# Optimization experiments

Measured on AMD Instinct MI355X. Metric: run time of the kernel, lower is better.

Reference implementation:

```python
import jax, jax.numpy as jnp
import numpy as np

B, FEAT, SPD_H, CTRL_H, N_CMD = 32768, 512, 128, 256, 4


def _p(key, shape, fan_in):
    # torch nn.Linear default init: U(-1/sqrt(fan_in), 1/sqrt(fan_in))
    lim = 1.0 / np.sqrt(fan_in)
    return jax.random.uniform(key, shape, jnp.float32, -lim, lim)


def setup_inputs() -> dict:
    key = jax.random.key(0)
    ks = iter(jax.random.split(key, 32))
    inp = {
        "feat": jax.random.normal(next(ks), (B, FEAT), jnp.float32),
        "speed": jax.random.uniform(next(ks), (B,), jnp.float32),
        "command": jax.random.randint(next(ks), (B,), 0, N_CMD, jnp.int32),
        "ms_w1": _p(next(ks), (1, SPD_H), 1), "ms_b1": _p(next(ks), (SPD_H,), 1),
        "ms_w2": _p(next(ks), (SPD_H, SPD_H), SPD_H), "ms_b2": _p(next(ks), (SPD_H,), SPD_H),
        "ms_w3": _p(next(ks), (SPD_H, SPD_H), SPD_H), "ms_b3": _p(next(ks), (SPD_H,), SPD_H),
        # speed_pred_module: 512 -> 256 -> 256 -> 1
        "sp_w1": _p(next(ks), (FEAT, CTRL_H), FEAT), "sp_b1": _p(next(ks), (CTRL_H,), FEAT),
        "sp_w2": _p(next(ks), (CTRL_H, CTRL_H), CTRL_H), "sp_b2": _p(next(ks), (CTRL_H,), CTRL_H),
        "sp_w3": _p(next(ks), (CTRL_H, 1), CTRL_H), "sp_b3": _p(next(ks), (1,), CTRL_H),
        # join_module: Linear(640, 512)
        "join_w": _p(next(ks), (FEAT + SPD_H, FEAT), FEAT + SPD_H),
        "join_b": _p(next(ks), (FEAT,), FEAT + SPD_H),
        # 4 control heads: 512 -> 256 -> 256 -> 3 (stacked on expert axis e)
        "ctrl_w1": _p(next(ks), (N_CMD, FEAT, CTRL_H), FEAT), "ctrl_b1": _p(next(ks), (N_CMD, CTRL_H), FEAT),
        "ctrl_w2": _p(next(ks), (N_CMD, CTRL_H, CTRL_H), CTRL_H), "ctrl_b2": _p(next(ks), (N_CMD, CTRL_H), CTRL_H),
        "ctrl_w3": _p(next(ks), (N_CMD, CTRL_H, 3), CTRL_H), "ctrl_b3": _p(next(ks), (N_CMD, 3), CTRL_H),
    }
    return inp


def _mlp(x, w1, b1, w2, b2, w3, b3):
    # FullyConnectedNet: Linear, ReLU, Linear, Dropout(p=0 -> noop), ReLU, Linear
    h = jax.nn.relu(x @ w1 + b1)
    h = jax.nn.relu(h @ w2 + b2)
    return h @ w3 + b3


def reference(feat, speed, command,
              ms_w1, ms_b1, ms_w2, ms_b2, ms_w3, ms_b3,
              sp_w1, sp_b1, sp_w2, sp_b2, sp_w3, sp_b3,
              join_w, join_b,
              ctrl_w1, ctrl_b1, ctrl_w2, ctrl_b2, ctrl_w3, ctrl_b3):
    v = _mlp(speed[:, None], ms_w1, ms_b1, ms_w2, ms_b2, ms_w3, ms_b3)      # [B,128]
    joined = jnp.concatenate([feat, v], axis=1) @ join_w + join_b           # [B,512]
    v_p = _mlp(feat, sp_w1, sp_b1, sp_w2, sp_b2, sp_w3, sp_b3)              # [B,1]
    # command-indexed dispatch: compute all 4 heads densely, then select per sample
    h1 = jax.nn.relu(jnp.einsum('bd,edh->beh', joined, ctrl_w1) + ctrl_b1)  # [B,4,256]
    h2 = jax.nn.relu(jnp.einsum('beh,ehk->bek', h1, ctrl_w2) + ctrl_b2)     # [B,4,256]
    act_all = jnp.einsum('bek,eko->beo', h2, ctrl_w3) + ctrl_b3             # [B,4,3]
    action = jnp.take_along_axis(act_all, command[:, None, None].astype(jnp.int32), axis=1)[:, 0]  # [B,3]
    throttle = jax.nn.sigmoid(action[:, 0])
    steering = jnp.tanh(action[:, 1])
    brake = jax.nn.sigmoid(action[:, 2])
    return v_p, throttle, brake, steering
```

## Files before the change

kernel.cpp:

```cpp
#include <hip/hip_runtime.h>
#include <hip/hip_bf16.h>
#include <stdint.h>
#include <math.h>

#define BB 32768
#define FEAT 512
#define SPD_H 128
#define CTRL_H 256
#define NCMD 4

typedef __attribute__((ext_vector_type(8))) short bf16x8;
typedef __attribute__((ext_vector_type(4))) float f32x4;

__device__ __forceinline__ unsigned short f2bf(float f) {
  union { float f; uint32_t u; } v; v.f = f;
  uint32_t u = v.u;
  return (unsigned short)((u + 0x7fffu + ((u >> 16) & 1u)) >> 16);
}

__device__ __forceinline__ bf16x8 pack8(float4 a, float4 b) {
  bf16x8 r;
  r[0] = (short)f2bf(a.x); r[1] = (short)f2bf(a.y);
  r[2] = (short)f2bf(a.z); r[3] = (short)f2bf(a.w);
  r[4] = (short)f2bf(b.x); r[5] = (short)f2bf(b.y);
  r[6] = (short)f2bf(b.z); r[7] = (short)f2bf(b.w);
  return r;
}

__device__ __forceinline__ void async16(const unsigned short* g, unsigned short* l) {
  __builtin_amdgcn_global_load_lds(
      (const __attribute__((address_space(1))) unsigned int*)g,
      (__attribute__((address_space(3))) unsigned int*)l, 16, 0, 0);
}

__device__ __forceinline__ void gemm128(
    const unsigned short* __restrict__ A, int lda,
    const int* __restrict__ perm, int m_start, int m_cnt,
    const unsigned short* __restrict__ W, const float* __restrict__ bi,
    unsigned short* __restrict__ C, int ldc, int relu, int K, int mt, int nt) {
  extern __shared__ __align__(16) unsigned char dynsm[];
  unsigned short* As = (unsigned short*)dynsm;
  unsigned short* Bs = As + 128 * 32;

  const int m0 = mt * 128;
  if (m0 >= m_cnt) return;
  const int n0 = nt * 128;
  const int t = threadIdx.x;
  const int w = t >> 6, lane = t & 63;
  const int wm = w & 1, wn = w >> 1;

  f32x4 acc[4][4];
#pragma unroll
  for (int i = 0; i < 4; ++i)
#pragma unroll
    for (int j = 0; j < 4; ++j)
#pragma unroll
      for (int r = 0; r < 4; ++r) acc[i][j][r] = 0.f;

  const int fr = lane & 15;
  const int fk = (lane >> 4) * 8;

  const unsigned short* agp[2]; const unsigned short* bgp[2];
  unsigned short* al[2]; unsigned short* bl[2];
#pragma unroll
  for (int it = 0; it < 2; ++it) {
    int row = w * 32 + it * 16 + (lane >> 2);
    int seg8 = (lane & 3) * 8;
    int rl = m0 + row;
    if (rl >= m_cnt) rl = m_cnt - 1;
    int grow = perm ? perm[m_start + rl] : (m_start + rl);
    agp[it] = A + (size_t)grow * lda + seg8;
    bgp[it] = W + (size_t)(n0 + row) * K + seg8;
    al[it] = As + (w * 32 + it * 16) * 32;
    bl[it] = Bs + (w * 32 + it * 16) * 32;
  }

  for (int k0 = 0; k0 < K; k0 += 32) {
#pragma unroll
    for (int it = 0; it < 2; ++it) {
      async16(agp[it] + k0, al[it]);
      async16(bgp[it] + k0, bl[it]);
    }
    __syncthreads();
    bf16x8 af[4], bfv[4];
#pragma unroll
    for (int i = 0; i < 4; ++i)
      af[i] = *(const bf16x8*)(As + (wm * 64 + i * 16 + fr) * 32 + fk);
#pragma unroll
    for (int j = 0; j < 4; ++j)
      bfv[j] = *(const bf16x8*)(Bs + (wn * 64 + j * 16 + fr) * 32 + fk);
#pragma unroll
    for (int i = 0; i < 4; ++i)
#pragma unroll
      for (int j = 0; j < 4; ++j)
        acc[i][j] = __builtin_amdgcn_mfma_f32_16x16x32_bf16(af[i], bfv[j], acc[i][j], 0, 0, 0);
    __syncthreads();
  }

  const int rquad = (lane >> 4) * 4;
  const int cidx = lane & 15;

  float bv[4];
#pragma unroll
  for (int j = 0; j < 4; ++j) bv[j] = bi ? bi[n0 + wn * 64 + j * 16 + cidx] : 0.f;

  unsigned short (*bscr)[136] = (unsigned short(*)[136])dynsm;
#pragma unroll
  for (int c = 0; c < 4; ++c) {
    if (wm == (c >> 1)) {
#pragma unroll
      for (int j = 0; j < 4; ++j) {
#pragma unroll
        for (int ii = 0; ii < 2; ++ii) {
          int i = 2 * (c & 1) + ii;
          int lr = ii * 16 + rquad;
#pragma unroll
          for (int r = 0; r < 4; ++r) {
            float v = acc[i][j][r] + bv[j];
            if (relu) v = fmaxf(v, 0.f);
            bscr[lr + r][wn * 64 + j * 16 + cidx] = f2bf(v);
          }
        }
      }
    }
    __syncthreads();
#pragma unroll
    for (int q = 0; q < 2; ++q) {
      int sg = t + 256 * q;
      int lr = sg >> 4, cs = (sg & 15) * 8;
      int grow = m0 + c * 32 + lr;
      if (grow < m_cnt)
        *(bf16x8*)(C + (size_t)(m_start + grow) * ldc + (n0 + cs)) =
            *(const bf16x8*)(&bscr[lr][cs]);
    }
    __syncthreads();
  }
}

struct WSeg { const float* src; unsigned short* dst; int K; int N; int ldd; };
struct PrepArgs {
  WSeg s[12];
  int start[13];
  const float* join_w; unsigned short* wjbf;
  const int* cmd; int* wavecnt;
  const float* join_b; const float* ctrl_w1; const float* ctrl_b1; float* b_f;
};
__launch_bounds__(256)
__global__ void k_prep(PrepArgs a) {
  int bx = blockIdx.x, t = threadIdx.x;
  if (bx < 320) {
    int idx = bx * 256 + t;
    float4 f = *(const float4*)(a.join_w + (size_t)idx * 4);
    ushort4 o;
    o.x = f2bf(f.x); o.y = f2bf(f.y); o.z = f2bf(f.z); o.w = f2bf(f.w);
    *(ushort4*)(a.wjbf + (size_t)idx * 4) = o;
    return;
  }
  int rel = bx - 320;
  if (rel < a.start[12]) {
    __shared__ float tb[32][33];
    int si = 0;
    while (rel >= a.start[si + 1]) ++si;
    WSeg sg = a.s[si];
    int tile = rel - a.start[si];
    int tkx = sg.K >> 5;
    int tn = tile / tkx;
    int tk = tile - tn * tkx;
    int k0 = tk * 32, n0 = tn * 32;
    int tx = t & 31, ty = t >> 5;
#pragma unroll
    for (int j = 0; j < 4; ++j)
      tb[ty + j * 8][tx] = sg.src[(size_t)(k0 + ty + j * 8) * sg.N + n0 + tx];
    __syncthreads();
#pragma unroll
    for (int j = 0; j < 4; ++j)
      sg.dst[(size_t)(n0 + ty + j * 8) * sg.ldd + k0 + tx] = f2bf(tb[tx][ty + j * 8]);
    return;
  }
  rel -= a.start[12];
  if (rel < 128) {
    int i = rel * 256 + t;
    int c = a.cmd[i];
    int wid = i >> 6;
    int lane = t & 63;
#pragma unroll
    for (int cv = 0; cv < NCMD; ++cv) {
      unsigned long long m = __ballot(c == cv);
      if (lane == 0) a.wavecnt[cv * 512 + wid] = __popcll(m);
    }
    return;
  }
  int e = rel - 128;
  float s0 = a.ctrl_b1[e * 256 + t], s1 = 0.f, s2 = 0.f, s3 = 0.f;
  const float* w = a.ctrl_w1 + (size_t)e * 512 * 256 + t;
#pragma unroll 4
  for (int m = 0; m < 512; m += 4) {
    s0 = fmaf(a.join_b[m + 0], w[(size_t)(m + 0) * 256], s0);
    s1 = fmaf(a.join_b[m + 1], w[(size_t)(m + 1) * 256], s1);
    s2 = fmaf(a.join_b[m + 2], w[(size_t)(m + 2) * 256], s2);
    s3 = fmaf(a.join_b[m + 3], w[(size_t)(m + 3) * 256], s3);
  }
  a.b_f[e * 256 + t] = (s0 + s1) + (s2 + s3);
}

struct MidArgs {
  const int* cmd; const int* wavecnt; int* perm; int* offs;
  const unsigned short* c_w1t; const unsigned short* wjbf; unsigned short* wf_t;
  const float* speed;
  const float* ms_w1; const float* ms_b1;
  const unsigned short* ms_w2t; const float* ms_b2;
  const unsigned short* ms_w3t; const float* ms_b3;
  unsigned short* msout;
  int* tile_e; int* tile_r0; int* ntl;
};
__launch_bounds__(256)
__global__ void k_mid(MidArgs a) {
  int b = blockIdx.x, t = threadIdx.x;
  if (b >= 168) {
    extern __shared__ __align__(16) unsigned char dynsm[];
    unsigned short (*hw)[136] = (unsigned short(*)[136])dynsm;
    unsigned short* BsM = (unsigned short*)(dynsm + 128 * 136 * 2);
    const int m0 = (b - 168) * 128;
    const int w = t >> 6, lane = t & 63;
    const int wm = w & 1, wn = w >> 1;
    const int fr = lane & 15, fk = (lane >> 4) * 8;
    const int rquad = (lane >> 4) * 4, cidx = lane & 15;
    {
      int r = t >> 1, half = t & 1;
      float s = a.speed[m0 + r];
#pragma unroll
      for (int c0 = 0; c0 < 64; c0 += 4) {
        int c = half * 64 + c0;
        float4 wv = *(const float4*)(a.ms_w1 + c);
        float4 bv = *(const float4*)(a.ms_b1 + c);
        hw[r][c + 0] = f2bf(fmaxf(fmaf(s, wv.x, bv.x), 0.f));
        hw[r][c + 1] = f2bf(fmaxf(fmaf(s, wv.y, bv.y), 0.f));
        hw[r][c + 2] = f2bf(fmaxf(fmaf(s, wv.z, bv.z), 0.f));
        hw[r][c + 3] = f2bf(fmaxf(fmaf(s, wv.w, bv.w), 0.f));
      }
    }
    __syncthreads();
    for (int layer = 0; layer < 2; ++layer) {
      const unsigned short* Wt = layer ? a.ms_w3t : a.ms_w2t;
      const float* bb = layer ? a.ms_b3 : a.ms_b2;
      f32x4 acc[4][4];
#pragma unroll
      for (int i = 0; i < 4; ++i)
#pragma unroll
        for (int j = 0; j < 4; ++j)
#pragma unroll
          for (int r = 0; r < 4; ++r) acc[i][j][r] = 0.f;
      for (int k0 = 0; k0 < 128; k0 += 32) {
#pragma unroll
        for (int it = 0; it < 2; ++it) {
          int row = w * 32 + it * 16 + (lane >> 2);
          async16(Wt + (size_t)row * 128 + k0 + (lane & 3) * 8,
                  BsM + (w * 32 + it * 16) * 32);
        }
        __syncthreads();
        bf16x8 af[4], bfv[4];
#pragma unroll
        for (int i = 0; i < 4; ++i)
          af[i] = *(const bf16x8*)(&hw[wm * 64 + i * 16 + fr][k0 + fk]);
#pragma unroll
        for (int j = 0; j < 4; ++j)
          bfv[j] = *(const bf16x8*)(BsM + (wn * 64 + j * 16 + fr) * 32 + fk);
#pragma unroll
        for (int i = 0; i < 4; ++i)
#pragma unroll
          for (int j = 0; j < 4; ++j)
            acc[i][j] = __builtin_amdgcn_mfma_f32_16x16x32_bf16(af[i], bfv[j], acc[i][j], 0, 0, 0);
        __syncthreads();
      }
#pragma unroll
      for (int j = 0; j < 4; ++j) {
        int col = wn * 64 + j * 16 + cidx;
        float bv = bb[col];
#pragma unroll
        for (int i = 0; i < 4; ++i) {
          int row = wm * 64 + i * 16 + rquad;
#pragma unroll
          for (int r = 0; r < 4; ++r) {
            float v = acc[i][j][r] + bv;
            if (layer == 0) v = fmaxf(v, 0.f);
            hw[row + r][col] = f2bf(v);
          }
        }
      }
      __syncthreads();
    }
    {
      int r = t >> 1, half = t & 1;
#pragma unroll
      for (int c8 = 0; c8 < 8; ++c8)
        *(bf16x8*)(a.msout + (size_t)(m0 + r) * 128 + half * 64 + c8 * 8) =
            *(const bf16x8*)(&hw[r][half * 64 + c8 * 8]);
    }
    return;
  }
  if (b >= 128) {
    int idx = b - 128;
    int mt = idx & 7, nt = idx >> 3;
    gemm128(a.c_w1t, 512, nullptr, 0, 1024, a.wjbf, nullptr, a.wf_t, 640, 0, 512, mt, nt);
    return;
  }
  __shared__ int pf[NCMD][4];
  __shared__ int tot[NCMD];
  int c = t >> 6, lane = t & 63;
  int v[8]; int s = 0;
#pragma unroll
  for (int q = 0; q < 8; ++q) { v[q] = a.wavecnt[c * 512 + lane * 8 + q]; s += v[q]; }
  int p = s;
#pragma unroll
  for (int m = 1; m < 64; m <<= 1) { int o = __shfl_up(p, m, 64); if (lane >= m) p += o; }
  int excl = p - s;
  if (lane == 63) tot[c] = p;
  if (lane == ((4 * b) >> 3)) {
    int base_off = (4 * b) & 7;
    int run = excl;
#pragma unroll
    for (int q = 0; q < 8; ++q) {
      if (q >= base_off && q < base_off + 4) pf[c][q - base_off] = run;
      run += v[q];
    }
  }
  __syncthreads();
  int soffs[NCMD + 1];
  soffs[0] = 0;
#pragma unroll
  for (int e = 0; e < NCMD; ++e) soffs[e + 1] = soffs[e] + tot[e];
  if (b == 0 && t == 0)
    for (int e = 0; e <= NCMD; ++e) a.offs[e] = soffs[e];
  int i = b * 256 + t;
  int mc = a.cmd[i];
  int lwid = t >> 6;
  int rank = 0, base = 0;
#pragma unroll
  for (int cv = 0; cv < NCMD; ++cv) {
    unsigned long long m = __ballot(mc == cv);
    if (mc == cv) {
      rank = __popcll(m & ((1ull << lane) - 1ull));
      base = soffs[cv] + pf[cv][lwid];
    }
  }
  a.perm[base + rank] = i;

  if (b == 0) {
    int toff[NCMD + 1];
    toff[0] = 0;
#pragma unroll
    for (int ee = 0; ee < NCMD; ++ee) toff[ee + 1] = toff[ee] + ((tot[ee] + 63) >> 6);
    if (t == 0) a.ntl[0] = toff[NCMD];
    for (int ti = t; ti < toff[NCMD]; ti += 256) {
      int ee = 0;
      while (ti >= toff[ee + 1]) ++ee;
      a.tile_e[ti] = ee;
      a.tile_r0[ti] = soffs[ee] + (ti - toff[ee]) * 64;
    }
  }
}

struct TailArgs {
  const float* feat;
  const unsigned short* msout;
  const unsigned short* wf_t;  const float* b_f;
  const unsigned short* sp_w1t; const float* sp_b1;
  const unsigned short* c_w2t; const float* ctrl_b2;
  const unsigned short* sp_w2t; const float* sp_b2;
  const float* ctrl_w3; const float* ctrl_b3;
  const float* sp_w3; const float* sp_b3;
  const int* perm; const int* seg;
  const int* tile_e; const int* tile_r0; const int* ntl;
  float* out;
};
__launch_bounds__(256, 3)
__global__ void k_tail(TailArgs a) {
  extern __shared__ __align__(16) unsigned char dynsm[];
  unsigned short* As = (unsigned short*)dynsm;
  unsigned short* h1 = (unsigned short*)(dynsm + 16384);
  float* pscr = (float*)dynsm;

  const int t = threadIdx.x;
  const int w = t >> 6, lane = t & 63;
  const int fr = lane & 15, fcg = lane >> 4;
  const int rquad = fcg * 4, cidx = fr;
  const int row_s = t >> 2, sl = t & 3;

  int is_sp, e = 0, NC;
  const unsigned short *W1, *W2;
  const float *b1, *b2;
  int r0, rend;
  if (blockIdx.x < 512) {
    is_sp = 1; NC = 8;
    W1 = a.sp_w1t; W2 = a.sp_w2t; b1 = a.sp_b1; b2 = a.sp_b2;
    r0 = blockIdx.x * 64; rend = BB;
  } else {
    int ti = blockIdx.x - 512;
    if (ti >= a.ntl[0]) return;
    is_sp = 0; e = a.tile_e[ti]; NC = 10;
    W1 = a.wf_t + (size_t)e * 256 * 640;
    W2 = a.c_w2t + (size_t)e * 65536;
    b1 = a.b_f + e * 256; b2 = a.ctrl_b2 + e * 256;
    r0 = a.tile_r0[ti]; rend = a.seg[e + 1];
  }
  const int K = is_sp ? 512 : 640;

  const float* fsrc; const unsigned short* msrc;
  {
    int rl = r0 + row_s;
    if (rl >= rend) rl = rend - 1;
    int grow = is_sp ? rl : a.perm[rl];
    fsrc = a.feat + (size_t)grow * 512 + sl * 16;
    msrc = a.msout + (size_t)grow * 128 + sl * 16;
  }
  const int xr = row_s & 7;
  unsigned short* wp0 = As + row_s * 64 + (((2 * sl) ^ xr) << 3);
  unsigned short* wp1 = As + row_s * 64 + (((2 * sl + 1) ^ xr) << 3);

  const unsigned short* bp[4];
#pragma unroll
  for (int j = 0; j < 4; ++j)
    bp[j] = W1 + (size_t)(w * 64 + j * 16 + fr) * K + fcg * 8;

  f32x4 acc[4][4];
#pragma unroll
  for (int i = 0; i < 4; ++i)
#pragma unroll
    for (int j = 0; j < 4; ++j)
#pragma unroll
      for (int r = 0; r < 4; ++r) acc[i][j][r] = 0.f;

  float4 g0, g1, g2, g3; bf16x8 mv0, mv1;

#define LOADA(cc)                                                        \
  do {                                                                   \
    if ((cc) < 8) {                                                      \
      g0 = *(const float4*)(fsrc + (cc) * 64 + 0);                       \
      g1 = *(const float4*)(fsrc + (cc) * 64 + 4);                       \
      g2 = *(const float4*)(fsrc + (cc) * 64 + 8);                       \
      g3 = *(const float4*)(fsrc + (cc) * 64 + 12);                      \
    } else {                                                             \
      mv0 = *(const bf16x8*)(msrc + ((cc) - 8) * 64 + 0);                \
      mv1 = *(const bf16x8*)(msrc + ((cc) - 8) * 64 + 8);                \
    }                                                                    \
  } while (0)

#define WRITEA(cc, bufb)                                                 \
  do {                                                                   \
    bf16x8 s0_, s1_;                                                     \
    if ((cc) < 8) { s0_ = pack8(g0, g1); s1_ = pack8(g2, g3); }          \
    else { s0_ = mv0; s1_ = mv1; }                                       \
    *(bf16x8*)(wp0 + (bufb)) = s0_;                                      \
    *(bf16x8*)(wp1 + (bufb)) = s1_;                                      \
  } while (0)

  LOADA(0);
  WRITEA(0, 0);
  LOADA(1);
  __syncthreads();

  for (int c = 0; c < NC; ++c) {
    const int cr = (c & 1) * 4096;
    if (c + 1 < NC) WRITEA(c + 1, ((c + 1) & 1) * 4096);
    if (c + 2 < NC) LOADA(c + 2);
#pragma unroll
    for (int ks = 0; ks < 2; ++ks) {
      const int k0 = c * 64 + ks * 32;
      bf16x8 af[4], bv[4];
#pragma unroll
      for (int i = 0; i < 4; ++i)
        af[i] = *(const bf16x8*)(As + cr + (i * 16 + fr) * 64 +
                                 (((ks * 4 + fcg) ^ (fr & 7)) << 3));
#pragma unroll
      for (int j = 0; j < 4; ++j)
        bv[j] = *(const bf16x8*)(bp[j] + k0);
#pragma unroll
      for (int i = 0; i < 4; ++i)
#pragma unroll
        for (int j = 0; j < 4; ++j)
          acc[i][j] = __builtin_amdgcn_mfma_f32_16x16x32_bf16(af[i], bv[j], acc[i][j], 0, 0, 0);
    }
    __syncthreads();
  }
#undef LOADA
#undef WRITEA

#pragma unroll
  for (int j = 0; j < 4; ++j) {
    const int col = w * 64 + j * 16 + cidx;
    const float bj = b1[col];
    const int c8 = col >> 3, cl = col & 7;
#pragma unroll
    for (int i = 0; i < 4; ++i) {
#pragma unroll
      for (int r = 0; r < 4; ++r) {
        const int row = i * 16 + rquad + r;
        h1[(row << 8) + (((c8 ^ (row & 7)) << 3) | cl)] =
            f2bf(fmaxf(acc[i][j][r] + bj, 0.f));
      }
    }
  }
  __syncthreads();

  const unsigned short* bp2[4];
#pragma unroll
  for (int j = 0; j < 4; ++j)
    bp2[j] = W2 + (size_t)(w * 64 + j * 16 + fr) * 256 + fcg * 8;

#pragma unroll
  for (int i = 0; i < 4; ++i)
#pragma unroll
    for (int j = 0; j < 4; ++j)
#pragma unroll
      for (int r = 0; r < 4; ++r) acc[i][j][r] = 0.f;

#pragma unroll 2
  for (int k0 = 0; k0 < 256; k0 += 32) {
    bf16x8 af[4], bv[4];
#pragma unroll
    for (int i = 0; i < 4; ++i) {
      const int row = i * 16 + fr;
      const int c8 = (k0 >> 3) + fcg;
      af[i] = *(const bf16x8*)(h1 + (row << 8) + ((c8 ^ (row & 7)) << 3));
    }
#pragma unroll
    for (int j = 0; j < 4; ++j)
      bv[j] = *(const bf16x8*)(bp2[j] + k0);
#pragma unroll
    for (int i = 0; i < 4; ++i)
#pragma unroll
      for (int j = 0; j < 4; ++j)
        acc[i][j] = __builtin_amdgcn_mfma_f32_16x16x32_bf16(af[i], bv[j], acc[i][j], 0, 0, 0);
  }

  float b2v[4], w30[4], w31[4], w32[4];
#pragma unroll
  for (int j = 0; j < 4; ++j) {
    const int col = w * 64 + j * 16 + cidx;
    b2v[j] = b2[col];
    if (is_sp) {
      w30[j] = a.sp_w3[col]; w31[j] = 0.f; w32[j] = 0.f;
    } else {
      const float* wp = a.ctrl_w3 + (size_t)e * 768 + col * 3;
      w30[j] = wp[0]; w31[j] = wp[1]; w32[j] = wp[2];
    }
  }
#pragma unroll
  for (int i = 0; i < 4; ++i) {
#pragma unroll
    for (int r = 0; r < 4; ++r) {
      float s0 = 0.f, s1 = 0.f, s2 = 0.f;
#pragma unroll
      for (int j = 0; j < 4; ++j) {
        const float v = fmaxf(acc[i][j][r] + b2v[j], 0.f);
        s0 = fmaf(v, w30[j], s0);
        if (!is_sp) { s1 = fmaf(v, w31[j], s1); s2 = fmaf(v, w32[j], s2); }
      }
#pragma unroll
      for (int m = 1; m <= 8; m <<= 1) {
        s0 += __shfl_xor(s0, m, 64);
        if (!is_sp) { s1 += __shfl_xor(s1, m, 64); s2 += __shfl_xor(s2, m, 64); }
      }
      if (cidx == 0) {
        const int row = i * 16 + rquad + r;
        pscr[(row * 4 + w) * 3 + 0] = s0;
        if (!is_sp) {
          pscr[(row * 4 + w) * 3 + 1] = s1;
          pscr[(row * 4 + w) * 3 + 2] = s2;
        }
      }
    }
  }
  __syncthreads();

  if (is_sp) {
    if (t < 64) {
      float s = pscr[t * 12] + pscr[t * 12 + 3] + pscr[t * 12 + 6] + pscr[t * 12 + 9]
              + a.sp_b3[0];
      a.out[r0 + t] = s;
    }
  } else {
    if (t < 192) {
      const int row = t / 3, o = t - row * 3;
      const int rl = r0 + row;
      if (rl < rend) {
        float s = pscr[row * 12 + o] + pscr[row * 12 + 3 + o] +
                  pscr[row * 12 + 6 + o] + pscr[row * 12 + 9 + o] +
                  a.ctrl_b3[e * 3 + o];
        const int orig = a.perm[rl];
        if (o == 0)      a.out[BB + orig]     = 1.f / (1.f + __expf(-s));
        else if (o == 2) a.out[2 * BB + orig] = 1.f / (1.f + __expf(-s));
        else             a.out[3 * BB + orig] = tanhf(s);
      }
    }
  }
}

static inline size_t align256(size_t x) { return (x + 255) & ~(size_t)255; }

extern "C" void kernel_launch(void* const* d_in, const int* in_sizes, int n_in,
                              void* d_out, int out_size, void* d_ws, size_t ws_size,
                              hipStream_t stream) {
  const float* feat   = (const float*)d_in[0];
  const float* speed  = (const float*)d_in[1];
  const int*   command= (const int*)d_in[2];
  const float* ms_w1  = (const float*)d_in[3];
  const float* ms_b1  = (const float*)d_in[4];
  const float* ms_w2  = (const float*)d_in[5];
  const float* ms_b2  = (const float*)d_in[6];
  const float* ms_w3  = (const float*)d_in[7];
  const float* ms_b3  = (const float*)d_in[8];
  const float* sp_w1  = (const float*)d_in[9];
  const float* sp_b1  = (const float*)d_in[10];
  const float* sp_w2  = (const float*)d_in[11];
  const float* sp_b2  = (const float*)d_in[12];
  const float* sp_w3  = (const float*)d_in[13];
  const float* sp_b3  = (const float*)d_in[14];
  const float* join_w = (const float*)d_in[15];
  const float* join_b = (const float*)d_in[16];
  const float* ctrl_w1= (const float*)d_in[17];
  const float* ctrl_b1= (const float*)d_in[18];
  const float* ctrl_w2= (const float*)d_in[19];
  const float* ctrl_b2= (const float*)d_in[20];
  const float* ctrl_w3= (const float*)d_in[21];
  const float* ctrl_b3= (const float*)d_in[22];
  float* out = (float*)d_out;

  char* ws = (char*)d_ws;
  size_t off = 0;
  auto alloc = [&](size_t bytes) -> char* { char* p = ws + off; off = align256(off + bytes); return p; };

  unsigned short* msout  = (unsigned short*)alloc((size_t)BB * 128 * 2);
  unsigned short* wtp    = (unsigned short*)alloc(1998848ull * 2);
  int* perm    = (int*)alloc((size_t)BB * 4);
  int* cnt     = (int*)alloc(64);
  int* wavecnt = (int*)alloc(4 * 512 * 4);
  float* b_f   = (float*)alloc(4 * 256 * 4);
  int* tile_e  = (int*)alloc(1056 * 4);
  int* tile_r0 = (int*)alloc(1056 * 4);
  int* ntl     = (int*)alloc(64);

  unsigned short* sp_w1t = wtp;
  unsigned short* sp_w2t = wtp + 131072;
  unsigned short* ms_w2t = wtp + 196608;
  unsigned short* ms_w3t = wtp + 212992;
  unsigned short* c_w1t  = wtp + 229376;
  unsigned short* c_w2t  = wtp + 753664;
  unsigned short* wjbf   = wtp + 1015808;
  unsigned short* wf_t   = wtp + 1343488;

  PrepArgs P;
  P.s[0] = { sp_w1, sp_w1t, 512, 256, 512 };
  P.s[1] = { sp_w2, sp_w2t, 256, 256, 256 };
  P.s[2] = { ms_w2, ms_w2t, 128, 128, 128 };
  P.s[3] = { ms_w3, ms_w3t, 128, 128, 128 };
  for (int e = 0; e < 4; ++e) P.s[4 + e] = { ctrl_w1 + (size_t)e * 512 * 256, c_w1t + (size_t)e * 131072, 512, 256, 512 };
  for (int e = 0; e < 4; ++e) P.s[8 + e] = { ctrl_w2 + (size_t)e * 256 * 256, c_w2t + (size_t)e * 65536, 256, 256, 256 };
  P.start[0] = 0;
  for (int i = 0; i < 12; ++i)
    P.start[i + 1] = P.start[i] + (P.s[i].K >> 5) * (P.s[i].N >> 5);
  P.join_w = join_w; P.wjbf = wjbf;
  P.cmd = command; P.wavecnt = wavecnt;
  P.join_b = join_b; P.ctrl_w1 = ctrl_w1; P.ctrl_b1 = ctrl_b1; P.b_f = b_f;
  int prep_blocks = 320 + P.start[12] + 128 + 4;

  k_prep<<<prep_blocks, 256, 0, stream>>>(P);

  MidArgs Mi;
  Mi.cmd = command; Mi.wavecnt = wavecnt; Mi.perm = perm; Mi.offs = cnt + 4;
  Mi.c_w1t = c_w1t; Mi.wjbf = wjbf; Mi.wf_t = wf_t;
  Mi.speed = speed;
  Mi.ms_w1 = ms_w1; Mi.ms_b1 = ms_b1;
  Mi.ms_w2t = ms_w2t; Mi.ms_b2 = ms_b2;
  Mi.ms_w3t = ms_w3t; Mi.ms_b3 = ms_b3;
  Mi.msout = msout;
  Mi.tile_e = tile_e; Mi.tile_r0 = tile_r0; Mi.ntl = ntl;
  k_mid<<<168 + 256, 256, 128 * 136 * 2 + 128 * 32 * 2, stream>>>(Mi);

  TailArgs T;
  T.feat = feat; T.msout = msout;
  T.wf_t = wf_t; T.b_f = b_f;
  T.sp_w1t = sp_w1t; T.sp_b1 = sp_b1;
  T.c_w2t = c_w2t; T.ctrl_b2 = ctrl_b2;
  T.sp_w2t = sp_w2t; T.sp_b2 = sp_b2;
  T.ctrl_w3 = ctrl_w3; T.ctrl_b3 = ctrl_b3;
  T.sp_w3 = sp_w3; T.sp_b3 = sp_b3;
  T.perm = perm; T.seg = cnt + 4;
  T.tile_e = tile_e; T.tile_r0 = tile_r0; T.ntl = ntl;
  T.out = out;
  k_tail<<<dim3(512 + 516), 256, 49152, stream>>>(T);
}
```

Measured before the change: 230.0 us.

## Fuse speed-pred MLP into control-head tail tiles and split bias fold

The speed-prediction MLP now runs inside each control-head tile instead of in separate blocks. Each tile reuses its staged feat A-tiles for both the control GEMM and the speed-pred GEMM and writes v_p through the permutation. This halves the feat reads and removes 512 blocks from the tail launch. In exchange each block holds two accumulator sets and uses more LDS (80KB), so occupancy drops to 2 blocks per CU. Separately, the join_b·ctrl_w1 bias fold is split into 32 partial blocks whose results k_mid reduces, which shortens the serial tail of k_prep.

```diff
diff --git a/kernel.cpp b/kernel.cpp
--- a/kernel.cpp
+++ b/kernel.cpp
@@ -143,7 +143,7 @@
   int start[13];
   const float* join_w; unsigned short* wjbf;
   const int* cmd; int* wavecnt;
-  const float* join_b; const float* ctrl_w1; const float* ctrl_b1; float* b_f;
+  const float* join_b; const float* ctrl_w1; float* bf_part;
 };
 __launch_bounds__(256)
 __global__ void k_prep(PrepArgs a) {
@@ -190,17 +190,25 @@
     }
     return;
   }
-  int e = rel - 128;
-  float s0 = a.ctrl_b1[e * 256 + t], s1 = 0.f, s2 = 0.f, s3 = 0.f;
-  const float* w = a.ctrl_w1 + (size_t)e * 512 * 256 + t;
-#pragma unroll 4
-  for (int m = 0; m < 512; m += 4) {
-    s0 = fmaf(a.join_b[m + 0], w[(size_t)(m + 0) * 256], s0);
-    s1 = fmaf(a.join_b[m + 1], w[(size_t)(m + 1) * 256], s1);
-    s2 = fmaf(a.join_b[m + 2], w[(size_t)(m + 2) * 256], s2);
-    s3 = fmaf(a.join_b[m + 3], w[(size_t)(m + 3) * 256], s3);
-  }
-  a.b_f[e * 256 + t] = (s0 + s1) + (s2 + s3);
+  int idx = rel - 128;
+  int e = idx >> 3, ch = idx & 7;
+  const float* w = a.ctrl_w1 + (size_t)e * 512 * 256 + (size_t)ch * 64 * 256 + t;
+  const float* jb = a.join_b + ch * 64;
+  float s0 = 0.f, s1 = 0.f, s2 = 0.f, s3 = 0.f;
+  float s4 = 0.f, s5 = 0.f, s6 = 0.f, s7 = 0.f;
+#pragma unroll
+  for (int g = 0; g < 8; ++g) {
+    s0 = fmaf(jb[g * 8 + 0], w[(size_t)(g * 8 + 0) * 256], s0);
+    s1 = fmaf(jb[g * 8 + 1], w[(size_t)(g * 8 + 1) * 256], s1);
+    s2 = fmaf(jb[g * 8 + 2], w[(size_t)(g * 8 + 2) * 256], s2);
+    s3 = fmaf(jb[g * 8 + 3], w[(size_t)(g * 8 + 3) * 256], s3);
+    s4 = fmaf(jb[g * 8 + 4], w[(size_t)(g * 8 + 4) * 256], s4);
+    s5 = fmaf(jb[g * 8 + 5], w[(size_t)(g * 8 + 5) * 256], s5);
+    s6 = fmaf(jb[g * 8 + 6], w[(size_t)(g * 8 + 6) * 256], s6);
+    s7 = fmaf(jb[g * 8 + 7], w[(size_t)(g * 8 + 7) * 256], s7);
+  }
+  a.bf_part[(size_t)(e * 8 + ch) * 256 + t] =
+      ((s0 + s1) + (s2 + s3)) + ((s4 + s5) + (s6 + s7));
 }
 
 struct MidArgs {
@@ -211,11 +219,20 @@
   const unsigned short* ms_w2t; const float* ms_b2;
   const unsigned short* ms_w3t; const float* ms_b3;
   unsigned short* msout;
+  const float* bf_part; const float* ctrl_b1; float* b_f;
   int* tile_e; int* tile_r0; int* ntl;
 };
 __launch_bounds__(256)
 __global__ void k_mid(MidArgs a) {
   int b = blockIdx.x, t = threadIdx.x;
+  if (b >= 424) {
+    int e = b - 424;
+    float s = a.ctrl_b1[e * 256 + t];
+#pragma unroll
+    for (int ch = 0; ch < 8; ++ch) s += a.bf_part[(size_t)(e * 8 + ch) * 256 + t];
+    a.b_f[e * 256 + t] = s;
+    return;
+  }
   if (b >= 168) {
     extern __shared__ __align__(16) unsigned char dynsm[];
     unsigned short (*hw)[136] = (unsigned short(*)[136])dynsm;
@@ -373,12 +390,14 @@
   const int* tile_e; const int* tile_r0; const int* ntl;
   float* out;
 };
-__launch_bounds__(256, 3)
+__launch_bounds__(256, 2)
 __global__ void k_tail(TailArgs a) {
   extern __shared__ __align__(16) unsigned char dynsm[];
-  unsigned short* As = (unsigned short*)dynsm;
-  unsigned short* h1 = (unsigned short*)(dynsm + 16384);
-  float* pscr = (float*)dynsm;
+  unsigned short* As  = (unsigned short*)dynsm;
+  unsigned short* h1c = (unsigned short*)(dynsm + 16384);
+  unsigned short* h1s = (unsigned short*)(dynsm + 49152);
+  float* pscr_c = (float*)dynsm;
+  float* pscr_s = (float*)(dynsm + 4096);
 
   const int t = threadIdx.x;
   const int w = t >> 6, lane = t & 63;
@@ -386,30 +405,21 @@
   const int rquad = fcg * 4, cidx = fr;
   const int row_s = t >> 2, sl = t & 3;
 
-  int is_sp, e = 0, NC;
-  const unsigned short *W1, *W2;
-  const float *b1, *b2;
-  int r0, rend;
-  if (blockIdx.x < 512) {
-    is_sp = 1; NC = 8;
-    W1 = a.sp_w1t; W2 = a.sp_w2t; b1 = a.sp_b1; b2 = a.sp_b2;
-    r0 = blockIdx.x * 64; rend = BB;
-  } else {
-    int ti = blockIdx.x - 512;
-    if (ti >= a.ntl[0]) return;
-    is_sp = 0; e = a.tile_e[ti]; NC = 10;
-    W1 = a.wf_t + (size_t)e * 256 * 640;
-    W2 = a.c_w2t + (size_t)e * 65536;
-    b1 = a.b_f + e * 256; b2 = a.ctrl_b2 + e * 256;
-    r0 = a.tile_r0[ti]; rend = a.seg[e + 1];
-  }
-  const int K = is_sp ? 512 : 640;
+  const int ti = blockIdx.x;
+  if (ti >= a.ntl[0]) return;
+  const int e = a.tile_e[ti];
+  const int r0 = a.tile_r0[ti], rend = a.seg[e + 1];
+
+  const unsigned short* W1c = a.wf_t + (size_t)e * 256 * 640;
+  const unsigned short* W2c = a.c_w2t + (size_t)e * 65536;
+  const float* b1c = a.b_f + e * 256;
+  const float* b2c = a.ctrl_b2 + e * 256;
 
   const float* fsrc; const unsigned short* msrc;
   {
     int rl = r0 + row_s;
     if (rl >= rend) rl = rend - 1;
-    int grow = is_sp ? rl : a.perm[rl];
+    int grow = a.perm[rl];
     fsrc = a.feat + (size_t)grow * 512 + sl * 16;
     msrc = a.msout + (size_t)grow * 128 + sl * 16;
   }
@@ -417,18 +427,21 @@
   unsigned short* wp0 = As + row_s * 64 + (((2 * sl) ^ xr) << 3);
   unsigned short* wp1 = As + row_s * 64 + (((2 * sl + 1) ^ xr) << 3);
 
-  const unsigned short* bp[4];
-#pragma unroll
-  for (int j = 0; j < 4; ++j)
-    bp[j] = W1 + (size_t)(w * 64 + j * 16 + fr) * K + fcg * 8;
-
-  f32x4 acc[4][4];
+  const unsigned short* bpc[4]; const unsigned short* bps[4];
+#pragma unroll
+  for (int j = 0; j < 4; ++j) {
+    const int row = w * 64 + j * 16 + fr;
+    bpc[j] = W1c + (size_t)row * 640 + fcg * 8;
+    bps[j] = a.sp_w1t + (size_t)row * 512 + fcg * 8;
+  }
+
+  f32x4 accC[4][4], accS[4][4];
 #pragma unroll
   for (int i = 0; i < 4; ++i)
 #pragma unroll
     for (int j = 0; j < 4; ++j)
 #pragma unroll
-      for (int r = 0; r < 4; ++r) acc[i][j][r] = 0.f;
+      for (int r = 0; r < 4; ++r) { accC[i][j][r] = 0.f; accS[i][j][r] = 0.f; }
 
   float4 g0, g1, g2, g3; bf16x8 mv0, mv1;
 
@@ -459,10 +472,11 @@
   LOADA(1);
   __syncthreads();
 
-  for (int c = 0; c < NC; ++c) {
+#pragma unroll 2
+  for (int c = 0; c < 10; ++c) {
     const int cr = (c & 1) * 4096;
-    if (c + 1 < NC) WRITEA(c + 1, ((c + 1) & 1) * 4096);
-    if (c + 2 < NC) LOADA(c + 2);
+    if (c + 1 < 10) WRITEA(c + 1, ((c + 1) & 1) * 4096);
+    if (c + 2 < 10) LOADA(c + 2);
 #pragma unroll
     for (int ks = 0; ks < 2; ++ks) {
       const int k0 = c * 64 + ks * 32;
@@ -473,12 +487,23 @@
                                  (((ks * 4 + fcg) ^ (fr & 7)) << 3));
 #pragma unroll
       for (int j = 0; j < 4; ++j)
-        bv[j] = *(const bf16x8*)(bp[j] + k0);
+        bv[j] = *(const bf16x8*)(bpc[j] + k0);
 #pragma unroll
       for (int i = 0; i < 4; ++i)
 #pragma unroll
         for (int j = 0; j < 4; ++j)
-          acc[i][j] = __builtin_amdgcn_mfma_f32_16x16x32_bf16(af[i], bv[j], acc[i][j], 0, 0, 0);
+          accC[i][j] = __builtin_amdgcn_mfma_f32_16x16x32_bf16(af[i], bv[j], accC[i][j], 0, 0, 0);
+      if (c < 8) {
+        bf16x8 bs[4];
+#pragma unroll
+        for (int j = 0; j < 4; ++j)
+          bs[j] = *(const bf16x8*)(bps[j] + k0);
+#pragma unroll
+        for (int i = 0; i < 4; ++i)
+#pragma unroll
+          for (int j = 0; j < 4; ++j)
+            accS[i][j] = __builtin_amdgcn_mfma_f32_16x16x32_bf16(af[i], bs[j], accS[i][j], 0, 0, 0);
+      }
     }
     __syncthreads();
   }
@@ -488,110 +513,122 @@
 #pragma unroll
   for (int j = 0; j < 4; ++j) {
     const int col = w * 64 + j * 16 + cidx;
-    const float bj = b1[col];
+    const float bjc = b1c[col];
+    const float bjs = a.sp_b1[col];
     const int c8 = col >> 3, cl = col & 7;
 #pragma unroll
     for (int i = 0; i < 4; ++i) {
 #pragma unroll
       for (int r = 0; r < 4; ++r) {
         const int row = i * 16 + rquad + r;
-        h1[(row << 8) + (((c8 ^ (row & 7)) << 3) | cl)] =
-            f2bf(fmaxf(acc[i][j][r] + bj, 0.f));
+        const int off = (row << 8) + (((c8 ^ (row & 7)) << 3) | cl);
+        h1c[off] = f2bf(fmaxf(accC[i][j][r] + bjc, 0.f));
+        h1s[off] = f2bf(fmaxf(accS[i][j][r] + bjs, 0.f));
       }
     }
   }
   __syncthreads();
 
-  const unsigned short* bp2[4];
-#pragma unroll
-  for (int j = 0; j < 4; ++j)
-    bp2[j] = W2 + (size_t)(w * 64 + j * 16 + fr) * 256 + fcg * 8;
-
+  const unsigned short* bp2c[4]; const unsigned short* bp2s[4];
+#pragma unroll
+  for (int j = 0; j < 4; ++j) {
+    const int row = w * 64 + j * 16 + fr;
+    bp2c[j] = W2c + (size_t)row * 256 + fcg * 8;
+    bp2s[j] = a.sp_w2t + (size_t)row * 256 + fcg * 8;
+  }
 #pragma unroll
   for (int i = 0; i < 4; ++i)
 #pragma unroll
     for (int j = 0; j < 4; ++j)
 #pragma unroll
-      for (int r = 0; r < 4; ++r) acc[i][j][r] = 0.f;
+      for (int r = 0; r < 4; ++r) { accC[i][j][r] = 0.f; accS[i][j][r] = 0.f; }
 
 #pragma unroll 2
   for (int k0 = 0; k0 < 256; k0 += 32) {
-    bf16x8 af[4], bv[4];
+    bf16x8 afc[4], afs[4], bv[4], bs[4];
 #pragma unroll
     for (int i = 0; i < 4; ++i) {
       const int row = i * 16 + fr;
       const int c8 = (k0 >> 3) + fcg;
-      af[i] = *(const bf16x8*)(h1 + (row << 8) + ((c8 ^ (row & 7)) << 3));
-    }
-#pragma unroll
-    for (int j = 0; j < 4; ++j)
-      bv[j] = *(const bf16x8*)(bp2[j] + k0);
+      const int off = (row << 8) + ((c8 ^ (row & 7)) << 3);
+      afc[i] = *(const bf16x8*)(h1c + off);
+      afs[i] = *(const bf16x8*)(h1s + off);
+    }
+#pragma unroll
+    for (int j = 0; j < 4; ++j) {
+      bv[j] = *(const bf16x8*)(bp2c[j] + k0);
+      bs[j] = *(const bf16x8*)(bp2s[j] + k0);
+    }
 #pragma unroll
     for (int i = 0; i < 4; ++i)
 #pragma unroll
-      for (int j = 0; j < 4; ++j)
-        acc[i][j] = __builtin_amdgcn_mfma_f32_16x16x32_bf16(af[i], bv[j], acc[i][j], 0, 0, 0);
-  }
-
-  float b2v[4], w30[4], w31[4], w32[4];
+      for (int j = 0; j < 4; ++j) {
+        accC[i][j] = __builtin_amdgcn_mfma_f32_16x16x32_bf16(afc[i], bv[j], accC[i][j], 0, 0, 0);
+        accS[i][j] = __builtin_amdgcn_mfma_f32_16x16x32_bf16(afs[i], bs[j], accS[i][j], 0, 0, 0);
+      }
+  }
+
+  float b2vc[4], b2vs[4], w30[4], w31[4], w32[4], ws3[4];
 #pragma unroll
   for (int j = 0; j < 4; ++j) {
     const int col = w * 64 + j * 16 + cidx;
-    b2v[j] = b2[col];
-    if (is_sp) {
-      w30[j] = a.sp_w3[col]; w31[j] = 0.f; w32[j] = 0.f;
-    } else {
-      const float* wp = a.ctrl_w3 + (size_t)e * 768 + col * 3;
-      w30[j] = wp[0]; w31[j] = wp[1]; w32[j] = wp[2];
-    }
+    b2vc[j] = b2c[col];
+    b2vs[j] = a.sp_b2[col];
+    ws3[j] = a.sp_w3[col];
+    const float* wp = a.ctrl_w3 + (size_t)e * 768 + col * 3;
+    w30[j] = wp[0]; w31[j] = wp[1]; w32[j] = wp[2];
   }
 #pragma unroll
   for (int i = 0; i < 4; ++i) {
 #pragma unroll
     for (int r = 0; r < 4; ++r) {
-      float s0 = 0.f, s1 = 0.f, s2 = 0.f;
+      float s0 = 0.f, s1 = 0.f, s2 = 0.f, sv = 0.f;
 #pragma unroll
       for (int j = 0; j < 4; ++j) {
-        const float v = fmaxf(acc[i][j][r] + b2v[j], 0.f);
-        s0 = fmaf(v, w30[j], s0);
-        if (!is_sp) { s1 = fmaf(v, w31[j], s1); s2 = fmaf(v, w32[j], s2); }
+        const float vc = fmaxf(accC[i][j][r] + b2vc[j], 0.f);
+        s0 = fmaf(vc, w30[j], s0);
+        s1 = fmaf(vc, w31[j], s1);
+        s2 = fmaf(vc, w32[j], s2);
+        const float vs = fmaxf(accS[i][j][r] + b2vs[j], 0.f);
+        sv = fmaf(vs, ws3[j], sv);
       }
 #pragma unroll
       for (int m = 1; m <= 8; m <<= 1) {
         s0 += __shfl_xor(s0, m, 64);
-        if (!is_sp) { s1 += __shfl_xor(s1, m, 64); s2 += __shfl_xor(s2, m, 64); }
+        s1 += __shfl_xor(s1, m, 64);
+        s2 += __shfl_xor(s2, m, 64);
+        sv += __shfl_xor(sv, m, 64);
       }
       if (cidx == 0) {
         const int row = i * 16 + rquad + r;
-        pscr[(row * 4 + w) * 3 + 0] = s0;
-        if (!is_sp) {
-          pscr[(row * 4 + w) * 3 + 1] = s1;
-          pscr[(row * 4 + w) * 3 + 2] = s2;
-        }
+        pscr_c[(row * 4 + w) * 3 + 0] = s0;
+        pscr_c[(row * 4 + w) * 3 + 1] = s1;
+        pscr_c[(row * 4 + w) * 3 + 2] = s2;
+        pscr_s[row * 4 + w] = sv;
       }
     }
   }
   __syncthreads();
 
-  if (is_sp) {
-    if (t < 64) {
-      float s = pscr[t * 12] + pscr[t * 12 + 3] + pscr[t * 12 + 6] + pscr[t * 12 + 9]
-              + a.sp_b3[0];
-      a.out[r0 + t] = s;
-    }
-  } else {
-    if (t < 192) {
-      const int row = t / 3, o = t - row * 3;
-      const int rl = r0 + row;
-      if (rl < rend) {
-        float s = pscr[row * 12 + o] + pscr[row * 12 + 3 + o] +
-                  pscr[row * 12 + 6 + o] + pscr[row * 12 + 9 + o] +
-                  a.ctrl_b3[e * 3 + o];
-        const int orig = a.perm[rl];
-        if (o == 0)      a.out[BB + orig]     = 1.f / (1.f + __expf(-s));
-        else if (o == 2) a.out[2 * BB + orig] = 1.f / (1.f + __expf(-s));
-        else             a.out[3 * BB + orig] = tanhf(s);
-      }
+  if (t < 64) {
+    const int rl = r0 + t;
+    if (rl < rend) {
+      float s = pscr_s[t * 4 + 0] + pscr_s[t * 4 + 1] +
+                pscr_s[t * 4 + 2] + pscr_s[t * 4 + 3] + a.sp_b3[0];
+      a.out[a.perm[rl]] = s;
+    }
+  }
+  if (t < 192) {
+    const int row = t / 3, o = t - row * 3;
+    const int rl = r0 + row;
+    if (rl < rend) {
+      float s = pscr_c[row * 12 + o] + pscr_c[row * 12 + 3 + o] +
+                pscr_c[row * 12 + 6 + o] + pscr_c[row * 12 + 9 + o] +
+                a.ctrl_b3[e * 3 + o];
+      const int orig = a.perm[rl];
+      if (o == 0)      a.out[BB + orig]     = 1.f / (1.f + __expf(-s));
+      else if (o == 2) a.out[2 * BB + orig] = 1.f / (1.f + __expf(-s));
+      else             a.out[3 * BB + orig] = tanhf(s);
     }
   }
 }
@@ -635,6 +672,7 @@
   int* perm    = (int*)alloc((size_t)BB * 4);
   int* cnt     = (int*)alloc(64);
   int* wavecnt = (int*)alloc(4 * 512 * 4);
+  float* bf_part = (float*)alloc(4 * 8 * 256 * 4);
   float* b_f   = (float*)alloc(4 * 256 * 4);
   int* tile_e  = (int*)alloc(1056 * 4);
   int* tile_r0 = (int*)alloc(1056 * 4);
@@ -661,8 +699,8 @@
     P.start[i + 1] = P.start[i] + (P.s[i].K >> 5) * (P.s[i].N >> 5);
   P.join_w = join_w; P.wjbf = wjbf;
   P.cmd = command; P.wavecnt = wavecnt;
-  P.join_b = join_b; P.ctrl_w1 = ctrl_w1; P.ctrl_b1 = ctrl_b1; P.b_f = b_f;
-  int prep_blocks = 320 + P.start[12] + 128 + 4;
+  P.join_b = join_b; P.ctrl_w1 = ctrl_w1; P.bf_part = bf_part;
+  int prep_blocks = 320 + P.start[12] + 128 + 32;
 
   k_prep<<<prep_blocks, 256, 0, stream>>>(P);
 
@@ -674,8 +712,9 @@
   Mi.ms_w2t = ms_w2t; Mi.ms_b2 = ms_b2;
   Mi.ms_w3t = ms_w3t; Mi.ms_b3 = ms_b3;
   Mi.msout = msout;
+  Mi.bf_part = bf_part; Mi.ctrl_b1 = ctrl_b1; Mi.b_f = b_f;
   Mi.tile_e = tile_e; Mi.tile_r0 = tile_r0; Mi.ntl = ntl;
-  k_mid<<<168 + 256, 256, 128 * 136 * 2 + 128 * 32 * 2, stream>>>(Mi);
+  k_mid<<<168 + 256 + 4, 256, 128 * 136 * 2 + 128 * 32 * 2, stream>>>(Mi);
 
   TailArgs T;
   T.feat = feat; T.msout = msout;
@@ -688,5 +727,5 @@
   T.perm = perm; T.seg = cnt + 4;
   T.tile_e = tile_e; T.tile_r0 = tile_r0; T.ntl = ntl;
   T.out = out;
-  k_tail<<<dim3(512 + 516), 256, 49152, stream>>>(T);
+  k_tail<<<dim3(520), 256, 81920, stream>>>(T);
 }
```

After: 242.3 us. +5.3%, slower.
